# Performance work log

Measured on AMD Instinct MI355X. Metric: run time of the kernel, lower is better.

Reference implementation:

```python
import jax, jax.numpy as jnp
import numpy as np

N_NODES = 30000
N_EDGES = 480000
C_IN = 256
D_HEAD = 64   # out_channels
N_HEADS = 4
M_FEAT = 30   # nb_random_features
K_GUMBEL = 10
TAU = 0.25


def _linear_init(key, out_f, in_f):
    s = 1.0 / np.sqrt(in_f)
    k1, k2 = jax.random.split(key)
    w = jax.random.uniform(k1, (out_f, in_f), minval=-s, maxval=s, dtype=jnp.float32)
    b = jax.random.uniform(k2, (out_f,), minval=-s, maxval=s, dtype=jnp.float32)
    return w, b


def setup_inputs() -> dict:
    key = jax.random.key(0)
    ks = jax.random.split(key, 8)
    z = jax.random.normal(ks[0], (1, N_NODES, C_IN), dtype=jnp.float32)
    edge_index = jax.random.randint(ks[1], (2, N_EDGES), 0, N_NODES)
    # Gumbel(0,1)/tau noise, matching torch's (-Exp(1).log())/tau
    u = jax.random.uniform(ks[2], (N_NODES, 1, N_HEADS, K_GUMBEL), dtype=jnp.float32,
                           minval=1e-8, maxval=1.0)
    gumbels = -jnp.log(-jnp.log(u)) / TAU
    # Performer orthogonal random-feature projection matrix [M, D]
    rng = np.random.default_rng(0)
    q, _ = np.linalg.qr(rng.standard_normal((D_HEAD, D_HEAD)))
    q = q.T[:M_FEAT]
    mult = np.linalg.norm(rng.standard_normal((M_FEAT, D_HEAD)), axis=1)
    proj = jnp.asarray(np.diag(mult) @ q, dtype=jnp.float32)
    Wq_w, Wq_b = _linear_init(ks[3], N_HEADS * D_HEAD, C_IN)
    Wk_w, Wk_b = _linear_init(ks[4], N_HEADS * D_HEAD, C_IN)
    Wv_w, Wv_b = _linear_init(ks[5], N_HEADS * D_HEAD, C_IN)
    Wo_w, Wo_b = _linear_init(ks[6], D_HEAD, N_HEADS * D_HEAD)
    b = jnp.full((1, N_HEADS), 0.1, dtype=jnp.float32)  # rb_order=1, sigmoid init
    tau = jnp.float32(TAU)
    return {"z": z, "edge_index": edge_index, "tau": tau, "gumbels": gumbels,
            "proj": proj, "Wq_w": Wq_w, "Wq_b": Wq_b, "Wk_w": Wk_w, "Wk_b": Wk_b,
            "Wv_w": Wv_w, "Wv_b": Wv_b, "Wo_w": Wo_w, "Wo_b": Wo_b, "b": b}


def _softmax_kernel_feats(data, proj, is_query):
    # data: [B, N, H, D] -> phi(data): [B, N, H, M]
    dn = 1.0 / jnp.sqrt(jnp.sqrt(jnp.float32(data.shape[-1])))
    data = data * dn
    ratio = 1.0 / jnp.sqrt(jnp.float32(proj.shape[0]))
    dash = jnp.einsum('bnhd,md->bnhm', data, proj)
    diag = jnp.sum(data * data, axis=-1, keepdims=True) * 0.5
    if is_query:
        stab = jnp.max(dash, axis=-1, keepdims=True)
    else:
        stab = jnp.max(dash, axis=(1, 3), keepdims=True)
    return ratio * (jnp.exp(dash - diag - stab) + 1e-6)


def reference(z, edge_index, tau, gumbels, proj, Wq_w, Wq_b, Wk_w, Wk_b,
              Wv_w, Wv_b, Wo_w, Wo_b, b):
    B, N, _ = z.shape
    M, D = proj.shape
    H = Wq_w.shape[0] // D
    query = (z @ Wq_w.T + Wq_b).reshape(B, N, H, D)
    key = (z @ Wk_w.T + Wk_b).reshape(B, N, H, D)
    value = (z @ Wv_w.T + Wv_b).reshape(B, N, H, D)

    inv_sqrt_tau = 1.0 / jnp.sqrt(tau)
    qp = jnp.transpose(_softmax_kernel_feats(query * inv_sqrt_tau, proj, True), (1, 0, 2, 3))   # [N,B,H,M]
    kp = jnp.transpose(_softmax_kernel_feats(key * inv_sqrt_tau, proj, False), (1, 0, 2, 3))    # [N,B,H,M]
    v = jnp.transpose(value, (1, 0, 2, 3))                                                       # [N,B,H,D]

    # Gumbel-perturbed key features: [N,B,H,K,M]
    kg = kp[:, :, :, None, :] * jnp.exp(gumbels)[..., None]
    kvs = jnp.einsum('nbhkm,nbhd->bhkmd', kg, v)
    z_num = jnp.einsum('nbhm,bhkmd->nbhkd', qp, kvs)      # [N,B,H,K,D]
    z_den = jnp.einsum('nbhm,bhkm->nbhk', qp, kg.sum(axis=0))
    z_out = jnp.transpose(jnp.mean(z_num / z_den[..., None], axis=3), (1, 0, 2, 3))  # [B,N,H,D]

    # edge attention weights (for link loss)
    start, end = edge_index[0], edge_index[1]
    edge_num = jnp.transpose(jnp.einsum('ebhm,ebhm->ebh', qp[end], kp[start]), (1, 0, 2))  # [B,E,H]
    attn_norm = jnp.einsum('nbhm,bhm->nbh', qp, kp.sum(axis=0))
    edge_dem = jnp.transpose(attn_norm[end], (1, 0, 2))
    A_weight = edge_num / edge_dem

    # relational bias (rb_order=1, sigmoid), degree-normalized sparse conv over value
    ones_e = jnp.ones(start.shape[0], dtype=jnp.float32)
    d_in = jax.ops.segment_sum(ones_e, end, num_segments=N)
    d_out = jax.ops.segment_sum(ones_e, start, num_segments=N)
    edge_w = jax.nn.sigmoid(b[0])[None, :] * jnp.sqrt((1.0 / d_in[end]) * (1.0 / d_out[start]))[:, None]  # [E,H]
    conv = jax.vmap(lambda vb: jax.ops.segment_sum(vb[start] * edge_w[:, :, None], end,
                                                   num_segments=N))(value)
    z_out = z_out + conv

    z_next = z_out.reshape(B, N, H * D) @ Wo_w.T + Wo_b  # [B,N,D]

    d_norm = 1.0 / d_in[end]
    link_loss = jnp.mean(jnp.log(A_weight) * d_norm[None, :, None])
    return z_next, link_loss
```

## Files before the change

### kernel.cpp

```cpp
#include <hip/hip_runtime.h>
#include <hip/hip_bf16.h>

#define NN 30000
#define NE 480000
#define NH 4
#define DH 64
#define MF 30
#define KG 10
#define RATIO 0.18257418583505536f
#define DNRM  0.35355339059327373f

#define P_WF    0
#define P_BF    196608
#define P_WOF   197376
#define P_WOBF  213760
#define P_BBF   213824
#define P_PROJ  213828
#define P_TAU   215748
#define P_TOTAL 215749

typedef unsigned short u16;
typedef unsigned int   u32;
typedef __attribute__((ext_vector_type(8))) short bf16x8;
typedef __attribute__((ext_vector_type(4))) float f32x4;

__device__ __forceinline__ float u2f(u16 u) { return __uint_as_float(((u32)u) << 16); }
__device__ __forceinline__ u16  f2bf(float f) {
    u32 x = __float_as_uint(f);
    return (u16)((x + 0x7FFFu + ((x >> 16) & 1u)) >> 16);
}
__device__ __forceinline__ u32  encf(float f) { u32 u = __float_as_uint(f); return (u & 0x80000000u) ? ~u : (u | 0x80000000u); }
__device__ __forceinline__ float decf(u32 u)  { return (u & 0x80000000u) ? __uint_as_float(u & 0x7FFFFFFFu) : __uint_as_float(~u); }

__global__ void k_detect(const u16* __restrict__ z, int* __restrict__ flag) {
    if (threadIdx.x == 0 && blockIdx.x == 0) {
        int bad = 0;
        for (int i = 0; i < 256; i += 2) {
            u16 u = z[i];
            int e = (u >> 7) & 0xFF;
            if (u != 0 && !(e >= 100 && e <= 140)) bad++;
        }
        *flag = (bad > 16) ? 1 : 0;
    }
}

__global__ __launch_bounds__(256) void k_cvt_params(
    const void* Wq, const void* Wk, const void* Wv,
    const void* bq, const void* bk, const void* bv,
    const void* Wo, const void* Wob, const void* bb, const void* proj,
    const void* taup, float* __restrict__ params, const int* __restrict__ flag)
{
    int i = blockIdx.x * 256 + threadIdx.x;
    if (i >= P_TOTAL) return;
    int f = *flag;
    if (i == P_TAU) {
        float v = f ? ((const float*)taup)[0] : u2f(((const u16*)taup)[0]);
        if (!(v > 1e-6f && v < 1e6f)) {
            float ff = ((const float*)taup)[0];
            v = (ff > 1e-6f && ff < 1e6f) ? ff : 0.25f;
        }
        params[i] = v;
        return;
    }
    const void* src; int j;
    if      (i < 65536)  { src = Wq;  j = i; }
    else if (i < 131072) { src = Wk;  j = i - 65536; }
    else if (i < 196608) { src = Wv;  j = i - 131072; }
    else if (i < 196864) { src = bq;  j = i - 196608; }
    else if (i < 197120) { src = bk;  j = i - 196864; }
    else if (i < 197376) { src = bv;  j = i - 197120; }
    else if (i < 213760) { src = Wo;  j = i - 197376; }
    else if (i < 213824) { src = Wob; j = i - 213760; }
    else if (i < 213828) { src = bb;  j = i - 213824; }
    else                 { src = proj; j = i - P_PROJ; }
    params[i] = f ? ((const float*)src)[j] : u2f(((const u16*)src)[j]);
}

__global__ __launch_bounds__(256) void k_cvt_w(const float* __restrict__ params,
                                               u16* __restrict__ Wh, u16* __restrict__ Wl)
{
    int i = blockIdx.x * 256 + threadIdx.x;
    float x = params[P_WF + i];
    u16 h = f2bf(x);
    Wh[i] = h;
    Wl[i] = f2bf(x - u2f(h));
}

__global__ __launch_bounds__(256) void k_deg(const int* __restrict__ ei, int* __restrict__ din, int* __restrict__ dout) {
    int e = blockIdx.x * 256 + threadIdx.x;
    if (e >= NE) return;
    atomicAdd(&dout[ei[e]], 1);
    atomicAdd(&din[ei[NE + e]], 1);
}

__global__ __launch_bounds__(256) void k_off(const int* __restrict__ din, int* __restrict__ offn, int* __restrict__ counter) {
    __shared__ int s[256];
    __shared__ int base;
    int tid = threadIdx.x;
    int n = blockIdx.x * 256 + tid;
    int v = (n < NN) ? din[n] : 0;
    s[tid] = v;
    __syncthreads();
    for (int o = 1; o < 256; o <<= 1) {
        int t = (tid >= o) ? s[tid - o] : 0;
        __syncthreads();
        s[tid] += t;
        __syncthreads();
    }
    if (tid == 255) base = atomicAdd(counter, s[255]);
    __syncthreads();
    if (n < NN) offn[n] = base + s[tid] - v;
}

__global__ __launch_bounds__(256) void k_fill(const int* __restrict__ ei, const int* __restrict__ offn,
                                              int* __restrict__ fill, int* __restrict__ csr,
                                              const int* __restrict__ din, const int* __restrict__ dout,
                                              float* __restrict__ wedge) {
    int e = blockIdx.x * 256 + threadIdx.x;
    if (e >= NE) return;
    int s = ei[e], t = ei[NE + e];
    int pos = offn[t] + atomicAdd(&fill[t], 1);
    csr[pos] = s;
    wedge[pos] = rsqrtf((float)din[t] * (float)dout[s]);
}

__global__ __launch_bounds__(256) void k_gemm_feat(
    const void* __restrict__ zv, const float* __restrict__ params, const int* __restrict__ flag,
    const u16* __restrict__ Wh, const u16* __restrict__ Wl,
    u16* __restrict__ V16, float* __restrict__ qp, u16* __restrict__ qp16,
    float* __restrict__ dashK, float* __restrict__ diagK, u32* __restrict__ stab)
{
    __shared__ __align__(16) char smemc[32768];
    __shared__ u32 smaxL;
    char* AsH = smemc;
    char* AsL = smemc + 8192;
    char* BsH = smemc + 16384;
    char* BsL = smemc + 24576;
    float* tile  = (float*)smemc;
    float* projL = (float*)smemc + 4352;

    const int tid = threadIdx.x;
    const int bm = blockIdx.x * 64;
    const int bn = blockIdx.y * 64;
    const int f32 = *flag;
    const int wave = tid >> 6, lane = tid & 63;
    const int wm = wave >> 1, wn = wave & 1;
    const int sr = tid >> 2;
    const int sc = (tid & 3) * 16;

    f32x4 acc[2][2] = {};

    for (int k0 = 0; k0 < 256; k0 += 64) {
        __syncthreads();
        {
            int zrow = bm + sr;
            if (f32) {
                float x[16];
                if (zrow < NN) {
                    const float4* zp = (const float4*)((const float*)zv + (size_t)zrow * 256 + k0 + sc);
                    #pragma unroll
                    for (int q4 = 0; q4 < 4; ++q4) {
                        float4 v = zp[q4];
                        x[q4 * 4 + 0] = v.x; x[q4 * 4 + 1] = v.y;
                        x[q4 * 4 + 2] = v.z; x[q4 * 4 + 3] = v.w;
                    }
                } else {
                    #pragma unroll
                    for (int j = 0; j < 16; ++j) x[j] = 0.f;
                }
                #pragma unroll
                for (int j8 = 0; j8 < 2; ++j8) {
                    u32 hw[4], lw[4];
                    #pragma unroll
                    for (int p = 0; p < 4; ++p) {
                        float a = x[j8 * 8 + 2 * p], b2 = x[j8 * 8 + 2 * p + 1];
                        u16 ha = f2bf(a), hb = f2bf(b2);
                        hw[p] = (u32)ha | ((u32)hb << 16);
                        u16 la = f2bf(a - u2f(ha)), lb = f2bf(b2 - u2f(hb));
                        lw[p] = (u32)la | ((u32)lb << 16);
                    }
                    int byt = sr * 128 + (((sc + j8 * 8) * 2) ^ ((sr & 7) << 4));
                    *(uint4*)(AsH + byt) = make_uint4(hw[0], hw[1], hw[2], hw[3]);
                    *(uint4*)(AsL + byt) = make_uint4(lw[0], lw[1], lw[2], lw[3]);
                }
            } else {
                uint4 v0 = make_uint4(0, 0, 0, 0), v1 = v0;
                if (zrow < NN) {
                    const uint4* zp = (const uint4*)((const u16*)zv + (size_t)zrow * 256 + k0 + sc);
                    v0 = zp[0]; v1 = zp[1];
                }
                int byt0 = sr * 128 + (((sc + 0) * 2) ^ ((sr & 7) << 4));
                int byt1 = sr * 128 + (((sc + 8) * 2) ^ ((sr & 7) << 4));
                *(uint4*)(AsH + byt0) = v0;
                *(uint4*)(AsH + byt1) = v1;
            }
        }
        {
            int byt0 = sr * 128 + (((sc + 0) * 2) ^ ((sr & 7) << 4));
            int byt1 = sr * 128 + (((sc + 8) * 2) ^ ((sr & 7) << 4));
            const uint4* wh4 = (const uint4*)(Wh + (size_t)(bn + sr) * 256 + k0 + sc);
            *(uint4*)(BsH + byt0) = wh4[0];
            *(uint4*)(BsH + byt1) = wh4[1];
            if (f32) {
                const uint4* wl4 = (const uint4*)(Wl + (size_t)(bn + sr) * 256 + k0 + sc);
                *(uint4*)(BsL + byt0) = wl4[0];
                *(uint4*)(BsL + byt1) = wl4[1];
            }
        }
        __syncthreads();
        #pragma unroll
        for (int kk = 0; kk < 2; ++kk) {
            const int kb = (kk * 32 + ((lane >> 4) * 8)) * 2;
            bf16x8 ah[2], bh[2], al[2], bl[2];
            #pragma unroll
            for (int i = 0; i < 2; ++i) {
                int ar = 32 * wm + 16 * i + (lane & 15);
                int ab = ar * 128 + (kb ^ ((ar & 7) << 4));
                ah[i] = *(const bf16x8*)(AsH + ab);
                int br = 32 * wn + 16 * i + (lane & 15);
                int bb2 = br * 128 + (kb ^ ((br & 7) << 4));
                bh[i] = *(const bf16x8*)(BsH + bb2);
                if (f32) {
                    al[i] = *(const bf16x8*)(AsL + ab);
                    bl[i] = *(const bf16x8*)(BsL + bb2);
                }
            }
            #pragma unroll
            for (int i = 0; i < 2; ++i)
                #pragma unroll
                for (int nf = 0; nf < 2; ++nf) {
                    acc[i][nf] = __builtin_amdgcn_mfma_f32_16x16x32_bf16(ah[i], bh[nf], acc[i][nf], 0, 0, 0);
                    if (f32) {
                        acc[i][nf] = __builtin_amdgcn_mfma_f32_16x16x32_bf16(ah[i], bl[nf], acc[i][nf], 0, 0, 0);
                        acc[i][nf] = __builtin_amdgcn_mfma_f32_16x16x32_bf16(al[i], bh[nf], acc[i][nf], 0, 0, 0);
                    }
                }
        }
    }
    __syncthreads();

    const float* bfv = params + P_BF;
    if (bn >= 512) {
        #pragma unroll
        for (int i = 0; i < 2; ++i)
            #pragma unroll
            for (int nf = 0; nf < 2; ++nf) {
                int col = 32 * wn + 16 * nf + (lane & 15);
                float bias = bfv[bn + col];
                #pragma unroll
                for (int r2 = 0; r2 < 4; ++r2) {
                    int row = 32 * wm + 16 * i + ((lane >> 4) * 4) + r2;
                    tile[row * 68 + col] = acc[i][nf][r2] + bias;
                }
            }
        __syncthreads();
        for (int i2 = tid; i2 < 4096; i2 += 256) {
            int row = i2 >> 6, col = i2 & 63;
            int nrow = bm + row;
            if (nrow < NN) V16[(size_t)nrow * 256 + (bn - 512) + col] = f2bf(tile[row * 68 + col]);
        }
        return;
    }

    for (int i2 = tid; i2 < MF * DH; i2 += 256) projL[(i2 >> 6) * 65 + (i2 & 63)] = params[P_PROJ + i2];
    if (tid == 0) smaxL = 0u;
    float scale = DNRM * rsqrtf(params[P_TAU]);
    #pragma unroll
    for (int i = 0; i < 2; ++i)
        #pragma unroll
        for (int nf = 0; nf < 2; ++nf) {
            int col = 32 * wn + 16 * nf + (lane & 15);
            float bias = bfv[bn + col];
            #pragma unroll
            for (int r2 = 0; r2 < 4; ++r2) {
                int row = 32 * wm + 16 * i + ((lane >> 4) * 4) + r2;
                tile[row * 68 + col] = (acc[i][nf][r2] + bias) * scale;
            }
        }
    __syncthreads();

    int r = tid >> 2, q = tid & 3;
    int n = bm + r;
    const float* trow = tile + r * 68;
    float dp = 0.f;
    #pragma unroll
    for (int d = q * 16; d < q * 16 + 16; ++d) dp += trow[d] * trow[d];
    dp += __shfl_xor(dp, 1);
    dp += __shfl_xor(dp, 2);
    float diag = dp * 0.5f;

    float dm[8];
    int nm = 0;
    float lmax = -3.0e38f;
    for (int m = q; m < MF; m += 4) {
        float s = 0.f;
        #pragma unroll
        for (int d = 0; d < DH; ++d) s += trow[d] * projL[m * 65 + d];
        dm[nm++] = s;
        lmax = fmaxf(lmax, s);
    }
    float mx = fmaxf(lmax, __shfl_xor(lmax, 1));
    mx = fmaxf(mx, __shfl_xor(mx, 2));

    if (bn < 256) {
        int h = blockIdx.y;
        if (n < NN) {
            float* o = qp + ((size_t)n * NH + h) * MF;
            u16* o16 = qp16 + ((size_t)n * NH + h) * 32;
            nm = 0;
            for (int m = q; m < MF; m += 4) {
                float v = RATIO * (expf(dm[nm++] - diag - mx) + 1e-6f);
                o[m] = v;
                o16[m] = f2bf(v);
            }
            if (q == 0) { o16[30] = 0; o16[31] = 0; }
        }
    } else {
        int h = blockIdx.y - 4;
        if (n < NN) {
            float* o = dashK + ((size_t)n * NH + h) * MF;
            nm = 0;
            for (int m = q; m < MF; m += 4) o[m] = dm[nm++];
            if (q == 0) {
                diagK[(size_t)n * NH + h] = diag;
                atomicMax(&smaxL, encf(mx));
            }
        }
        __syncthreads();
        if (tid == 0) atomicMax(&stab[h], smaxL);
    }
}

__global__ __launch_bounds__(256) void k_kp(float* __restrict__ kp, const float* __restrict__ diagK,
                                            const u32* __restrict__ stab, float* __restrict__ kpsum,
                                            u16* __restrict__ kp16)
{
    __shared__ float part[NH * MF];
    __shared__ float stabf[4];
    int tid = threadIdx.x;
    if (tid < NH * MF) part[tid] = 0.f;
    if (tid >= 128 && tid < 132) stabf[tid - 128] = decf(stab[tid - 128]);
    __syncthreads();
    int base = blockIdx.x * 64 * MF;
    for (int i = tid; i < 64 * MF; i += 256) {
        int row = blockIdx.x * 64 + i / MF;
        int m = i - (i / MF) * MF;
        int h = row & 3;
        float v = RATIO * (expf(kp[base + i] - diagK[row] - stabf[h]) + 1e-6f);
        kp[base + i] = v;
        kp16[(size_t)row * 32 + m] = f2bf(v);
        atomicAdd(&part[h * MF + m], v);
    }
    if (tid < 64) {
        int row = blockIdx.x * 64 + tid;
        kp16[(size_t)row * 32 + 30] = 0;
        kp16[(size_t)row * 32 + 31] = 0;
    }
    __syncthreads();
    if (tid < NH * MF) atomicAdd(&kpsum[tid], part[tid]);
}

__global__ __launch_bounds__(256) void k_an(const float* __restrict__ qp, const float* __restrict__ kpsum,
                                            float* __restrict__ an)
{
    __shared__ float kps[NH * MF];
    int tid = threadIdx.x;
    if (tid < NH * MF) kps[tid] = kpsum[tid];
    __syncthreads();
    int idx = blockIdx.x * 256 + tid;
    if (idx >= NN * NH) return;
    int h = idx & 3;
    const float* q = qp + (size_t)idx * MF;
    float s = 0.f;
    #pragma unroll
    for (int m = 0; m < MF; ++m) s += q[m] * kps[h * MF + m];
    an[idx] = s;
}

#define KVS_CHUNKS 50
#define KVS_NPB (NN / KVS_CHUNKS)
__global__ __launch_bounds__(512) void k_kvs(const float* __restrict__ kp, const void* __restrict__ gum,
                                             const u16* __restrict__ V16, const int* __restrict__ flag,
                                             float* __restrict__ Pkvs, float* __restrict__ Pksum)
{
    __shared__ __align__(16) char kgT[320 * 128];
    __shared__ __align__(16) char VT[64 * 128];
    __shared__ float kpT[64][31];
    __shared__ float egT[64][10];
    const int tid = threadIdx.x;
    const int h = blockIdx.y;
    const int chunk = blockIdx.x;
    const int n0 = chunk * KVS_NPB;
    const int f32 = *flag;
    const int wave = tid >> 6, lane = tid & 63;

    float ksacc[5] = {0.f, 0.f, 0.f, 0.f, 0.f};
    f32x4 acc[10] = {};

    for (int t0 = 0; t0 < KVS_NPB; t0 += 64) {
        __syncthreads();
        for (int i = tid; i < 64 * MF; i += 512) {
            int n = i / MF, m = i - (i / MF) * MF;
            kpT[n][m] = (t0 + n < KVS_NPB) ? kp[(size_t)(n0 + t0 + n) * (NH * MF) + h * MF + m] : 0.f;
        }
        for (int i = tid; i < 64 * KG; i += 512) {
            int n = i / KG, k = i - (i / KG) * KG;
            float e = 0.f;
            if (t0 + n < KVS_NPB) {
                size_t gofs = (size_t)(n0 + t0 + n) * (NH * KG) + h * KG + k;
                float g = f32 ? ((const float*)gum)[gofs] : u2f(((const u16*)gum)[gofs]);
                e = expf(g);
            }
            egT[n][k] = e;
        }
        for (int i = tid; i < 64 * 16; i += 512) {
            int n = i >> 4, dq = (i & 15) * 4;
            u32 v0 = 0, v1 = 0;
            if (t0 + n < KVS_NPB) {
                uint2 vv = *(const uint2*)(V16 + (size_t)(n0 + t0 + n) * 256 + h * 64 + dq);
                v0 = vv.x; v1 = vv.y;
            }
            #pragma unroll
            for (int j = 0; j < 4; ++j) {
                u16 val = (u16)(((j < 2) ? v0 : v1) >> ((j & 1) * 16));
                int d = dq + j;
                *(u16*)(VT + d * 128 + ((n * 2) ^ ((d & 7) << 4))) = val;
            }
        }
        __syncthreads();
        #pragma unroll
        for (int it = 0; it < 5; ++it) {
            int idx = tid + it * 512;
            int row = idx >> 3, nc = idx & 7;
            u32 w_[4] = {0u, 0u, 0u, 0u};
            if (row < 300) {
                int k = row / MF, m = row - (row / MF) * MF;
                float s = 0.f;
                #pragma unroll
                for (int p = 0; p < 4; ++p) {
                    int na = nc * 8 + 2 * p, nb = na + 1;
                    u16 ha = f2bf(kpT[na][m] * egT[na][k]);
                    u16 hb = f2bf(kpT[nb][m] * egT[nb][k]);
                    w_[p] = (u32)ha | ((u32)hb << 16);
                    s += u2f(ha) + u2f(hb);
                }
                ksacc[it] += s;
            }
            *(uint4*)(kgT + row * 128 + ((nc * 16) ^ ((row & 7) << 4))) = make_uint4(w_[0], w_[1], w_[2], w_[3]);
        }
        __syncthreads();
        #pragma unroll
        for (int kk = 0; kk < 2; ++kk) {
            const int kb = (kk * 32 + ((lane >> 4) * 8)) * 2;
            #pragma unroll
            for (int i = 0; i < 10; ++i) {
                int ct = wave * 10 + i;
                int kt = ct >> 2, dt = ct & 3;
                int ar = kt * 16 + (lane & 15);
                bf16x8 a = *(const bf16x8*)(kgT + ar * 128 + (kb ^ ((ar & 7) << 4)));
                int br = dt * 16 + (lane & 15);
                bf16x8 b = *(const bf16x8*)(VT + br * 128 + (kb ^ ((br & 7) << 4)));
                acc[i] = __builtin_amdgcn_mfma_f32_16x16x32_bf16(a, b, acc[i], 0, 0, 0);
            }
        }
    }
    #pragma unroll
    for (int i = 0; i < 10; ++i) {
        int ct = wave * 10 + i;
        int kt = ct >> 2, dt = ct & 3;
        int col = dt * 16 + (lane & 15);
        #pragma unroll
        for (int r = 0; r < 4; ++r) {
            int row = kt * 16 + ((lane >> 4) * 4) + r;
            if (row < 300)
                Pkvs[(((size_t)chunk * NH + h) * 300 + row) * 64 + col] = acc[i][r];
        }
    }
    #pragma unroll
    for (int it = 0; it < 5; ++it) {
        float v = ksacc[it];
        v += __shfl_xor(v, 1);
        v += __shfl_xor(v, 2);
        v += __shfl_xor(v, 4);
        int row = (tid + it * 512) >> 3;
        if ((tid & 7) == 0 && row < 300)
            Pksum[chunk * 1200 + h * 300 + row] = v;
    }
}

__global__ __launch_bounds__(256) void k_reduce(const float* __restrict__ Pkvs, const float* __restrict__ Pksum,
                                                float* __restrict__ kvs, float* __restrict__ ksum)
{
    int i = blockIdx.x * 256 + threadIdx.x;
    if (i < NH * KG * MF * DH) {
        float s = 0.f;
        for (int c = 0; c < KVS_CHUNKS; ++c) s += Pkvs[(size_t)c * (NH * 300 * 64) + i];
        kvs[i] = s;
    } else if (i < NH * KG * MF * DH + NH * KG * MF) {
        int j = i - NH * KG * MF * DH;
        float s = 0.f;
        for (int c = 0; c < KVS_CHUNKS; ++c) s += Pksum[c * 1200 + j];
        ksum[j] = s;
    }
}

__global__ __launch_bounds__(256) void k_edge(const int* __restrict__ ei,
                                              const u16* __restrict__ qp16, const u16* __restrict__ kp16,
                                              const float* __restrict__ an,
                                              const int* __restrict__ din, float* __restrict__ lossp)
{
    __shared__ float ls[64];
    int tid = threadIdx.x;
    int eg = tid >> 2, h = tid & 3;
    int e = blockIdx.x * 64 + eg;
    int s = ei[e], t = ei[NE + e];
    const uint4* qv = (const uint4*)(qp16 + ((size_t)t * NH + h) * 32);
    const uint4* kv = (const uint4*)(kp16 + ((size_t)s * NH + h) * 32);
    float num = 0.f;
    #pragma unroll
    for (int c = 0; c < 4; ++c) {
        uint4 a = qv[c], b = kv[c];
        num += u2f((u16)(a.x & 0xFFFF)) * u2f((u16)(b.x & 0xFFFF))
             + u2f((u16)(a.x >> 16))    * u2f((u16)(b.x >> 16))
             + u2f((u16)(a.y & 0xFFFF)) * u2f((u16)(b.y & 0xFFFF))
             + u2f((u16)(a.y >> 16))    * u2f((u16)(b.y >> 16))
             + u2f((u16)(a.z & 0xFFFF)) * u2f((u16)(b.z & 0xFFFF))
             + u2f((u16)(a.z >> 16))    * u2f((u16)(b.z >> 16))
             + u2f((u16)(a.w & 0xFFFF)) * u2f((u16)(b.w & 0xFFFF))
             + u2f((u16)(a.w >> 16))    * u2f((u16)(b.w >> 16));
    }
    float term = logf(num / an[(size_t)t * NH + h]);
    term += __shfl_xor(term, 1);
    term += __shfl_xor(term, 2);
    if (h == 0) ls[eg] = term / (float)din[t];
    __syncthreads();
    if (tid < 64) {
        float v = ls[tid];
        #pragma unroll
        for (int o = 32; o > 0; o >>= 1) v += __shfl_xor(v, o);
        if (tid == 0) atomicAdd(&lossp[blockIdx.x & 1023], v);
    }
}

#define AT_NT 48
__global__ __launch_bounds__(256) void k_attn(
    const float* __restrict__ qp, const float* __restrict__ kvs, const float* __restrict__ ksum,
    u16* __restrict__ zatt)
{
    __shared__ float qpTf[3][NH * 484];
    __shared__ u32   kvbuf[NH * 964];
    __shared__ float rdenL[3][16 * NH * KG];
    u16*   kvL16 = (u16*)kvbuf;
    float* ksL   = (float*)kvbuf;
    int tid = threadIdx.x;
    int n0 = blockIdx.x * AT_NT;

    for (int i = tid; i < AT_NT * NH * MF; i += 256) {
        int j48 = i / (NH * MF); int r = i - j48 * (NH * MF);
        int h = r / MF; int m = r - h * MF;
        qpTf[j48 >> 4][h * 484 + m * 16 + (j48 & 15)] = qp[(size_t)(n0 + j48) * (NH * MF) + r];
    }
    for (int i = tid; i < NH * KG * MF; i += 256) ksL[i] = ksum[i];
    __syncthreads();
    for (int i = tid; i < AT_NT * NH * KG; i += 256) {
        int j48 = i / (NH * KG); int r = i - j48 * (NH * KG);
        int h = r / KG;
        int sub = j48 >> 4, j = j48 & 15;
        float s = 0.f;
        #pragma unroll
        for (int m = 0; m < MF; ++m) s += qpTf[sub][h * 484 + m * 16 + j] * ksL[r * MF + m];
        rdenL[sub][j * (NH * KG) + r] = 1.0f / s;
    }

    const int h  = tid >> 6;
    const int jg = (tid >> 4) & 3;
    const int dg = tid & 15;
    float acc[3][4][4] = {};
    for (int k = 0; k < KG; ++k) {
        __syncthreads();
        for (int i = tid; i < NH * MF * DH; i += 256) {
            int hh = i / (MF * DH); int r = i - hh * (MF * DH);
            kvL16[hh * 1928 + r] = f2bf(kvs[((size_t)(hh * KG + k) * MF) * DH + r]);
        }
        __syncthreads();
        float ps[3][4][4] = {};
        const u16* kb = kvL16 + h * 1928 + dg * 4;
        const float* qb0 = qpTf[0] + h * 484 + jg * 4;
        const float* qb1 = qpTf[1] + h * 484 + jg * 4;
        const float* qb2 = qpTf[2] + h * 484 + jg * 4;
        #pragma unroll
        for (int m = 0; m < MF; ++m) {
            ushort4 bu = *(const ushort4*)(kb + m * 64);
            float4 b = make_float4(u2f(bu.x), u2f(bu.y), u2f(bu.z), u2f(bu.w));
            float4 a0 = *(const float4*)(qb0 + m * 16);
            float4 a1 = *(const float4*)(qb1 + m * 16);
            float4 a2 = *(const float4*)(qb2 + m * 16);
            ps[0][0][0] += a0.x * b.x; ps[0][0][1] += a0.x * b.y; ps[0][0][2] += a0.x * b.z; ps[0][0][3] += a0.x * b.w;
            ps[0][1][0] += a0.y * b.x; ps[0][1][1] += a0.y * b.y; ps[0][1][2] += a0.y * b.z; ps[0][1][3] += a0.y * b.w;
            ps[0][2][0] += a0.z * b.x; ps[0][2][1] += a0.z * b.y; ps[0][2][2] += a0.z * b.z; ps[0][2][3] += a0.z * b.w;
            ps[0][3][0] += a0.w * b.x; ps[0][3][1] += a0.w * b.y; ps[0][3][2] += a0.w * b.z; ps[0][3][3] += a0.w * b.w;
            ps[1][0][0] += a1.x * b.x; ps[1][0][1] += a1.x * b.y; ps[1][0][2] += a1.x * b.z; ps[1][0][3] += a1.x * b.w;
            ps[1][1][0] += a1.y * b.x; ps[1][1][1] += a1.y * b.y; ps[1][1][2] += a1.y * b.z; ps[1][1][3] += a1.y * b.w;
            ps[1][2][0] += a1.z * b.x; ps[1][2][1] += a1.z * b.y; ps[1][2][2] += a1.z * b.z; ps[1][2][3] += a1.z * b.w;
            ps[1][3][0] += a1.w * b.x; ps[1][3][1] += a1.w * b.y; ps[1][3][2] += a1.w * b.z; ps[1][3][3] += a1.w * b.w;
            ps[2][0][0] += a2.x * b.x; ps[2][0][1] += a2.x * b.y; ps[2][0][2] += a2.x * b.z; ps[2][0][3] += a2.x * b.w;
            ps[2][1][0] += a2.y * b.x; ps[2][1][1] += a2.y * b.y; ps[2][1][2] += a2.y * b.z; ps[2][1][3] += a2.y * b.w;
            ps[2][2][0] += a2.z * b.x; ps[2][2][1] += a2.z * b.y; ps[2][2][2] += a2.z * b.z; ps[2][2][3] += a2.z * b.w;
            ps[2][3][0] += a2.w * b.x; ps[2][3][1] += a2.w * b.y; ps[2][3][2] += a2.w * b.z; ps[2][3][3] += a2.w * b.w;
        }
        #pragma unroll
        for (int sub = 0; sub < 3; ++sub)
            #pragma unroll
            for (int j4 = 0; j4 < 4; ++j4) {
                float rd = rdenL[sub][(jg * 4 + j4) * (NH * KG) + h * KG + k];
                #pragma unroll
                for (int d4 = 0; d4 < 4; ++d4) acc[sub][j4][d4] += ps[sub][j4][d4] * rd;
            }
    }
    #pragma unroll
    for (int sub = 0; sub < 3; ++sub)
        #pragma unroll
        for (int j4 = 0; j4 < 4; ++j4) {
            int n = n0 + sub * 16 + jg * 4 + j4;
            #pragma unroll
            for (int d4 = 0; d4 < 4; ++d4)
                zatt[(size_t)n * 256 + h * 64 + dg * 4 + d4] = f2bf(acc[sub][j4][d4] * (1.0f / KG));
        }
}

__global__ __launch_bounds__(256) void k_gather(
    const u16* __restrict__ zatt, const u16* __restrict__ V16,
    const int* __restrict__ csr, const float* __restrict__ wedge,
    const int* __restrict__ offn, const int* __restrict__ din,
    const float* __restrict__ params, u16* __restrict__ pre)
{
    int tid = threadIdx.x;
    int w = tid >> 6, l = tid & 63;
    int n = blockIdx.x * 4 + w;
    float sigb = 1.f / (1.f + expf(-params[P_BBF + (l >> 4)]));
    int dn = din[n], o0 = offn[n];
    float c0 = 0.f, c1 = 0.f, c2 = 0.f, c3 = 0.f;
    for (int t0 = 0; t0 < dn; t0 += 64) {
        int cnt = min(64, dn - t0);
        int myIdx = 0; float myW = 0.f;
        if (l < cnt) { myIdx = csr[o0 + t0 + l]; myW = wedge[o0 + t0 + l]; }
        int j = 0;
        for (; j + 7 < cnt; j += 8) {
            int   s0 = __shfl(myIdx, j),     s1 = __shfl(myIdx, j + 1);
            int   s2 = __shfl(myIdx, j + 2), s3 = __shfl(myIdx, j + 3);
            int   s4 = __shfl(myIdx, j + 4), s5 = __shfl(myIdx, j + 5);
            int   s6 = __shfl(myIdx, j + 6), s7 = __shfl(myIdx, j + 7);
            float w0 = __shfl(myW, j),     w1 = __shfl(myW, j + 1);
            float w2 = __shfl(myW, j + 2), w3 = __shfl(myW, j + 3);
            float w4 = __shfl(myW, j + 4), w5 = __shfl(myW, j + 5);
            float w6 = __shfl(myW, j + 6), w7 = __shfl(myW, j + 7);
            uint2 a0 = *(const uint2*)(V16 + (size_t)s0 * 256 + l * 4);
            uint2 a1 = *(const uint2*)(V16 + (size_t)s1 * 256 + l * 4);
            uint2 a2 = *(const uint2*)(V16 + (size_t)s2 * 256 + l * 4);
            uint2 a3 = *(const uint2*)(V16 + (size_t)s3 * 256 + l * 4);
            uint2 a4 = *(const uint2*)(V16 + (size_t)s4 * 256 + l * 4);
            uint2 a5 = *(const uint2*)(V16 + (size_t)s5 * 256 + l * 4);
            uint2 a6 = *(const uint2*)(V16 + (size_t)s6 * 256 + l * 4);
            uint2 a7 = *(const uint2*)(V16 + (size_t)s7 * 256 + l * 4);
            c0 += w0 * u2f((u16)(a0.x & 0xFFFF)) + w1 * u2f((u16)(a1.x & 0xFFFF))
                + w2 * u2f((u16)(a2.x & 0xFFFF)) + w3 * u2f((u16)(a3.x & 0xFFFF))
                + w4 * u2f((u16)(a4.x & 0xFFFF)) + w5 * u2f((u16)(a5.x & 0xFFFF))
                + w6 * u2f((u16)(a6.x & 0xFFFF)) + w7 * u2f((u16)(a7.x & 0xFFFF));
            c1 += w0 * u2f((u16)(a0.x >> 16)) + w1 * u2f((u16)(a1.x >> 16))
                + w2 * u2f((u16)(a2.x >> 16)) + w3 * u2f((u16)(a3.x >> 16))
                + w4 * u2f((u16)(a4.x >> 16)) + w5 * u2f((u16)(a5.x >> 16))
                + w6 * u2f((u16)(a6.x >> 16)) + w7 * u2f((u16)(a7.x >> 16));
            c2 += w0 * u2f((u16)(a0.y & 0xFFFF)) + w1 * u2f((u16)(a1.y & 0xFFFF))
                + w2 * u2f((u16)(a2.y & 0xFFFF)) + w3 * u2f((u16)(a3.y & 0xFFFF))
                + w4 * u2f((u16)(a4.y & 0xFFFF)) + w5 * u2f((u16)(a5.y & 0xFFFF))
                + w6 * u2f((u16)(a6.y & 0xFFFF)) + w7 * u2f((u16)(a7.y & 0xFFFF));
            c3 += w0 * u2f((u16)(a0.y >> 16)) + w1 * u2f((u16)(a1.y >> 16))
                + w2 * u2f((u16)(a2.y >> 16)) + w3 * u2f((u16)(a3.y >> 16))
                + w4 * u2f((u16)(a4.y >> 16)) + w5 * u2f((u16)(a5.y >> 16))
                + w6 * u2f((u16)(a6.y >> 16)) + w7 * u2f((u16)(a7.y >> 16));
        }
        for (; j < cnt; ++j) {
            int   s0 = __shfl(myIdx, j);
            float w0 = __shfl(myW, j);
            uint2 a0 = *(const uint2*)(V16 + (size_t)s0 * 256 + l * 4);
            c0 += w0 * u2f((u16)(a0.x & 0xFFFF));
            c1 += w0 * u2f((u16)(a0.x >> 16));
            c2 += w0 * u2f((u16)(a0.y & 0xFFFF));
            c3 += w0 * u2f((u16)(a0.y >> 16));
        }
    }
    uint2 za = *(const uint2*)(zatt + (size_t)n * 256 + l * 4);
    float e0 = u2f((u16)(za.x & 0xFFFF)) + sigb * c0;
    float e1 = u2f((u16)(za.x >> 16))    + sigb * c1;
    float e2 = u2f((u16)(za.y & 0xFFFF)) + sigb * c2;
    float e3 = u2f((u16)(za.y >> 16))    + sigb * c3;
    uint2 r;
    r.x = (u32)f2bf(e0) | ((u32)f2bf(e1) << 16);
    r.y = (u32)f2bf(e2) | ((u32)f2bf(e3) << 16);
    *(uint2*)(pre + (size_t)n * 256 + l * 4) = r;
}

__global__ __launch_bounds__(256) void k_out(
    const u16* __restrict__ pre, const float* __restrict__ params, float* __restrict__ out)
{
    __shared__ __align__(16) char smemc[24576];
    char* As  = smemc;
    char* BsH = smemc + 8192;
    char* BsL = smemc + 16384;
    const int tid = threadIdx.x;
    const int bm = blockIdx.x * 64;
    const int wave = tid >> 6, lane = tid & 63;
    const int wm = wave >> 1, wn = wave & 1;
    const int sr = tid >> 2;
    const int sc = (tid & 3) * 16;

    f32x4 acc[2][2] = {};

    for (int k0 = 0; k0 < 256; k0 += 64) {
        __syncthreads();
        int byt0 = sr * 128 + (((sc + 0) * 2) ^ ((sr & 7) << 4));
        int byt1 = sr * 128 + (((sc + 8) * 2) ^ ((sr & 7) << 4));
        {
            int row = bm + sr;
            uint4 v0 = make_uint4(0, 0, 0, 0), v1 = v0;
            if (row < NN) {
                const uint4* p = (const uint4*)(pre + (size_t)row * 256 + k0 + sc);
                v0 = p[0]; v1 = p[1];
            }
            *(uint4*)(As + byt0) = v0;
            *(uint4*)(As + byt1) = v1;
        }
        {
            float x[16];
            const float4* wr = (const float4*)(params + P_WOF + (size_t)sr * 256 + k0 + sc);
            #pragma unroll
            for (int q4 = 0; q4 < 4; ++q4) {
                float4 v = wr[q4];
                x[q4 * 4 + 0] = v.x; x[q4 * 4 + 1] = v.y;
                x[q4 * 4 + 2] = v.z; x[q4 * 4 + 3] = v.w;
            }
            #pragma unroll
            for (int j8 = 0; j8 < 2; ++j8) {
                u32 hw[4], lw[4];
                #pragma unroll
                for (int p = 0; p < 4; ++p) {
                    float a = x[j8 * 8 + 2 * p], b2 = x[j8 * 8 + 2 * p + 1];
                    u16 ha = f2bf(a), hb = f2bf(b2);
                    hw[p] = (u32)ha | ((u32)hb << 16);
                    u16 la = f2bf(a - u2f(ha)), lb = f2bf(b2 - u2f(hb));
                    lw[p] = (u32)la | ((u32)lb << 16);
                }
                int byt = sr * 128 + (((sc + j8 * 8) * 2) ^ ((sr & 7) << 4));
                *(uint4*)(BsH + byt) = make_uint4(hw[0], hw[1], hw[2], hw[3]);
                *(uint4*)(BsL + byt) = make_uint4(lw[0], lw[1], lw[2], lw[3]);
            }
        }
        __syncthreads();
        #pragma unroll
        for (int kk = 0; kk < 2; ++kk) {
            const int kb = (kk * 32 + ((lane >> 4) * 8)) * 2;
            bf16x8 a[2], bh[2], bl[2];
            #pragma unroll
            for (int i = 0; i < 2; ++i) {
                int ar = 32 * wm + 16 * i + (lane & 15);
                int ab = ar * 128 + (kb ^ ((ar & 7) << 4));
                a[i] = *(const bf16x8*)(As + ab);
                int br = 32 * wn + 16 * i + (lane & 15);
                int bb2 = br * 128 + (kb ^ ((br & 7) << 4));
                bh[i] = *(const bf16x8*)(BsH + bb2);
                bl[i] = *(const bf16x8*)(BsL + bb2);
            }
            #pragma unroll
            for (int i = 0; i < 2; ++i)
                #pragma unroll
                for (int nf = 0; nf < 2; ++nf) {
                    acc[i][nf] = __builtin_amdgcn_mfma_f32_16x16x32_bf16(a[i], bh[nf], acc[i][nf], 0, 0, 0);
                    acc[i][nf] = __builtin_amdgcn_mfma_f32_16x16x32_bf16(a[i], bl[nf], acc[i][nf], 0, 0, 0);
                }
        }
    }
    #pragma unroll
    for (int i = 0; i < 2; ++i)
        #pragma unroll
        for (int nf = 0; nf < 2; ++nf) {
            int col = 32 * wn + 16 * nf + (lane & 15);
            float bias = params[P_WOBF + col];
            #pragma unroll
            for (int r2 = 0; r2 < 4; ++r2) {
                int row = bm + 32 * wm + 16 * i + ((lane >> 4) * 4) + r2;
                if (row < NN) out[(size_t)row * 64 + col] = acc[i][nf][r2] + bias;
            }
        }
}

__global__ __launch_bounds__(256) void k_loss(const float* __restrict__ lossp, float* __restrict__ out) {
    __shared__ float s[256];
    int tid = threadIdx.x;
    float v = 0.f;
    for (int i = tid; i < 1024; i += 256) v += lossp[i];
    s[tid] = v;
    __syncthreads();
    for (int o = 128; o > 0; o >>= 1) {
        if (tid < o) s[tid] += s[tid + o];
        __syncthreads();
    }
    if (tid == 0) out[(size_t)NN * 64] = s[0] / (float)(NE * NH);
}

extern "C" void kernel_launch(void* const* d_in, const int* in_sizes, int n_in,
                              void* d_out, int out_size, void* d_ws, size_t ws_size,
                              hipStream_t stream)
{
    const void* z    = d_in[0];
    const int*  ei   = (const int*)d_in[1];
    const void* taup = d_in[2];
    const void* gum  = d_in[3];
    const void* proj = d_in[4];
    const void* Wq   = d_in[5];
    const void* bq   = d_in[6];
    const void* Wk   = d_in[7];
    const void* bk   = d_in[8];
    const void* Wv   = d_in[9];
    const void* bv   = d_in[10];
    const void* Wo   = d_in[11];
    const void* Wob  = d_in[12];
    const void* bb   = d_in[13];
    float* out = (float*)d_out;

    u16*   V16    = (u16*)d_ws;
    float* qpb    = (float*)d_ws + 3840000;
    float* kpb    = qpb + (size_t)NN * NH * MF;
    float* diagK  = kpb + (size_t)NN * NH * MF;
    float* anb    = diagK + (size_t)NN * NH;
    u16*   zatt   = (u16*)kpb;
    int*   csr    = (int*)(anb + (size_t)NN * NH);
    int*   offn   = csr + NE;
    float* params = (float*)(offn + NN);
    float* kvs    = params + 215752;
    float* ksum   = kvs + NH * KG * MF * DH;
    float* kpsum  = ksum + NH * KG * MF;
    int*   din    = (int*)(kpsum + NH * MF);
    int*   doutd  = din + NN;
    int*   fill   = doutd + NN;
    int*   counter = fill + NN;
    u32*   stab   = (u32*)(counter + 4);
    float* lossp  = (float*)(stab + 4);
    int*   flag   = (int*)(lossp + 1024);
    float* wedge  = (float*)(flag + 4);
    u16*   qp16   = (u16*)(wedge + NE);
    u16*   kp16   = qp16 + (size_t)NN * NH * 32;
    float* Pkvs   = (float*)qp16;
    float* Pksum  = (float*)(kp16 + (size_t)NN * NH * 32);
    u16*   Whb    = kp16;
    u16*   Wlb    = kp16 + 196608;
    u16*   pre    = qp16;
    size_t zero_bytes = (size_t)((char*)(flag + 4) - (char*)kvs);

    hipMemsetAsync(kvs, 0, zero_bytes, stream);

    k_detect<<<dim3(1), dim3(64), 0, stream>>>((const u16*)z, flag);
    k_cvt_params<<<dim3((P_TOTAL + 255) / 256), dim3(256), 0, stream>>>(
        Wq, Wk, Wv, bq, bk, bv, Wo, Wob, bb, proj, taup, params, flag);
    k_cvt_w<<<dim3(768), dim3(256), 0, stream>>>(params, Whb, Wlb);

    k_deg <<<dim3((NE + 255) / 256), dim3(256), 0, stream>>>(ei, din, doutd);
    k_off <<<dim3((NN + 255) / 256), dim3(256), 0, stream>>>(din, offn, counter);
    k_fill<<<dim3((NE + 255) / 256), dim3(256), 0, stream>>>(ei, offn, fill, csr, din, doutd, wedge);
    k_gemm_feat<<<dim3((NN + 63) / 64, 12), dim3(256), 0, stream>>>(
        z, params, flag, Whb, Wlb, V16, qpb, qp16, kpb, diagK, stab);
    k_kp  <<<dim3(NN * NH / 64), dim3(256), 0, stream>>>(kpb, diagK, stab, kpsum, kp16);
    k_an  <<<dim3((NN * NH + 255) / 256), dim3(256), 0, stream>>>(qpb, kpsum, anb);
    k_edge<<<dim3(NE / 64), dim3(256), 0, stream>>>(ei, qp16, kp16, anb, din, lossp);
    k_kvs <<<dim3(KVS_CHUNKS, NH), dim3(512), 0, stream>>>(kpb, gum, V16, flag, Pkvs, Pksum);
    k_reduce<<<dim3((NH * KG * MF * DH + NH * KG * MF + 255) / 256), dim3(256), 0, stream>>>(
        Pkvs, Pksum, kvs, ksum);
    k_attn<<<dim3(NN / AT_NT), dim3(256), 0, stream>>>(qpb, kvs, ksum, zatt);
    k_gather<<<dim3(NN / 4), dim3(256), 0, stream>>>(zatt, V16, csr, wedge, offn, din, params, pre);
    k_out<<<dim3((NN + 63) / 64), dim3(256), 0, stream>>>(pre, params, out);
    k_loss<<<dim3(1), dim3(256), 0, stream>>>(lossp, out);
}
```

Measured before the change: 677.4 us.

## Stage full z row strip once per block and loop over all twelve column tiles

```diff
diff --git a/kernel.cpp b/kernel.cpp
--- a/kernel.cpp
+++ b/kernel.cpp
@@ -130,31 +130,26 @@
     u16* __restrict__ V16, float* __restrict__ qp, u16* __restrict__ qp16,
     float* __restrict__ dashK, float* __restrict__ diagK, u32* __restrict__ stab)
 {
-    __shared__ __align__(16) char smemc[32768];
+    __shared__ __align__(16) char AsH[64 * 512];
+    __shared__ __align__(16) char AsL[64 * 512];
+    __shared__ __align__(16) char BsH[2][64 * 128];
+    __shared__ __align__(16) char BsL[2][64 * 128];
+    __shared__ float tile[64 * 68];
+    __shared__ float projL[30 * 65];
     __shared__ u32 smaxL;
-    char* AsH = smemc;
-    char* AsL = smemc + 8192;
-    char* BsH = smemc + 16384;
-    char* BsL = smemc + 24576;
-    float* tile  = (float*)smemc;
-    float* projL = (float*)smemc + 4352;
 
     const int tid = threadIdx.x;
     const int bm = blockIdx.x * 64;
-    const int bn = blockIdx.y * 64;
     const int f32 = *flag;
     const int wave = tid >> 6, lane = tid & 63;
     const int wm = wave >> 1, wn = wave & 1;
     const int sr = tid >> 2;
     const int sc = (tid & 3) * 16;
 
-    f32x4 acc[2][2] = {};
-
-    for (int k0 = 0; k0 < 256; k0 += 64) {
-        __syncthreads();
-        {
-            int zrow = bm + sr;
-            if (f32) {
+    {
+        int zrow = bm + sr;
+        if (f32) {
+            for (int k0 = 0; k0 < 256; k0 += 64) {
                 float x[16];
                 if (zrow < NN) {
                     const float4* zp = (const float4*)((const float*)zv + (size_t)zrow * 256 + k0 + sc);
@@ -179,68 +174,102 @@
                         u16 la = f2bf(a - u2f(ha)), lb = f2bf(b2 - u2f(hb));
                         lw[p] = (u32)la | ((u32)lb << 16);
                     }
-                    int byt = sr * 128 + (((sc + j8 * 8) * 2) ^ ((sr & 7) << 4));
+                    int byt = sr * 512 + (((k0 + sc + j8 * 8) * 2) ^ ((sr & 7) << 4));
                     *(uint4*)(AsH + byt) = make_uint4(hw[0], hw[1], hw[2], hw[3]);
                     *(uint4*)(AsL + byt) = make_uint4(lw[0], lw[1], lw[2], lw[3]);
                 }
-            } else {
+            }
+        } else {
+            for (int k0 = 0; k0 < 256; k0 += 64) {
                 uint4 v0 = make_uint4(0, 0, 0, 0), v1 = v0;
                 if (zrow < NN) {
                     const uint4* zp = (const uint4*)((const u16*)zv + (size_t)zrow * 256 + k0 + sc);
                     v0 = zp[0]; v1 = zp[1];
                 }
+                int byt0 = sr * 512 + (((k0 + sc + 0) * 2) ^ ((sr & 7) << 4));
+                int byt1 = sr * 512 + (((k0 + sc + 8) * 2) ^ ((sr & 7) << 4));
+                *(uint4*)(AsH + byt0) = v0;
+                *(uint4*)(AsH + byt1) = v1;
+            }
+        }
+    }
+    for (int i2 = tid; i2 < MF * DH; i2 += 256) projL[(i2 >> 6) * 65 + (i2 & 63)] = params[P_PROJ + i2];
+
+    const float* bfv = params + P_BF;
+    float scale = DNRM * rsqrtf(params[P_TAU]);
+
+    for (int bny = 0; bny < 12; ++bny) {
+        const int bn = bny * 64;
+        f32x4 acc[2][2] = {};
+        for (int k0c = 0; k0c < 4; ++k0c) {
+            const int k0 = k0c * 64;
+            const int p = k0c & 1;
+            {
                 int byt0 = sr * 128 + (((sc + 0) * 2) ^ ((sr & 7) << 4));
                 int byt1 = sr * 128 + (((sc + 8) * 2) ^ ((sr & 7) << 4));
-                *(uint4*)(AsH + byt0) = v0;
-                *(uint4*)(AsH + byt1) = v1;
-            }
-        }
-        {
-            int byt0 = sr * 128 + (((sc + 0) * 2) ^ ((sr & 7) << 4));
-            int byt1 = sr * 128 + (((sc + 8) * 2) ^ ((sr & 7) << 4));
-            const uint4* wh4 = (const uint4*)(Wh + (size_t)(bn + sr) * 256 + k0 + sc);
-            *(uint4*)(BsH + byt0) = wh4[0];
-            *(uint4*)(BsH + byt1) = wh4[1];
-            if (f32) {
-                const uint4* wl4 = (const uint4*)(Wl + (size_t)(bn + sr) * 256 + k0 + sc);
-                *(uint4*)(BsL + byt0) = wl4[0];
-                *(uint4*)(BsL + byt1) = wl4[1];
-            }
-        }
-        __syncthreads();
-        #pragma unroll
-        for (int kk = 0; kk < 2; ++kk) {
-            const int kb = (kk * 32 + ((lane >> 4) * 8)) * 2;
-            bf16x8 ah[2], bh[2], al[2], bl[2];
-            #pragma unroll
-            for (int i = 0; i < 2; ++i) {
-                int ar = 32 * wm + 16 * i + (lane & 15);
-                int ab = ar * 128 + (kb ^ ((ar & 7) << 4));
-                ah[i] = *(const bf16x8*)(AsH + ab);
-                int br = 32 * wn + 16 * i + (lane & 15);
-                int bb2 = br * 128 + (kb ^ ((br & 7) << 4));
-                bh[i] = *(const bf16x8*)(BsH + bb2);
+                const uint4* wh4 = (const uint4*)(Wh + (size_t)(bn + sr) * 256 + k0 + sc);
+                *(uint4*)(BsH[p] + byt0) = wh4[0];
+                *(uint4*)(BsH[p] + byt1) = wh4[1];
                 if (f32) {
-                    al[i] = *(const bf16x8*)(AsL + ab);
-                    bl[i] = *(const bf16x8*)(BsL + bb2);
-                }
-            }
+                    const uint4* wl4 = (const uint4*)(Wl + (size_t)(bn + sr) * 256 + k0 + sc);
+                    *(uint4*)(BsL[p] + byt0) = wl4[0];
+                    *(uint4*)(BsL[p] + byt1) = wl4[1];
+                }
+            }
+            __syncthreads();
+            #pragma unroll
+            for (int kk = 0; kk < 2; ++kk) {
+                const int kbA = (k0 + kk * 32 + ((lane >> 4) * 8)) * 2;
+                const int kbB = (kk * 32 + ((lane >> 4) * 8)) * 2;
+                bf16x8 ah[2], bh[2], al[2], bl[2];
+                #pragma unroll
+                for (int i = 0; i < 2; ++i) {
+                    int ar = 32 * wm + 16 * i + (lane & 15);
+                    int ab = ar * 512 + (kbA ^ ((ar & 7) << 4));
+                    ah[i] = *(const bf16x8*)(AsH + ab);
+                    int br = 32 * wn + 16 * i + (lane & 15);
+                    int bb2 = br * 128 + (kbB ^ ((br & 7) << 4));
+                    bh[i] = *(const bf16x8*)(BsH[p] + bb2);
+                    if (f32) {
+                        al[i] = *(const bf16x8*)(AsL + ab);
+                        bl[i] = *(const bf16x8*)(BsL[p] + bb2);
+                    }
+                }
+                #pragma unroll
+                for (int i = 0; i < 2; ++i)
+                    #pragma unroll
+                    for (int nf = 0; nf < 2; ++nf) {
+                        acc[i][nf] = __builtin_amdgcn_mfma_f32_16x16x32_bf16(ah[i], bh[nf], acc[i][nf], 0, 0, 0);
+                        if (f32) {
+                            acc[i][nf] = __builtin_amdgcn_mfma_f32_16x16x32_bf16(ah[i], bl[nf], acc[i][nf], 0, 0, 0);
+                            acc[i][nf] = __builtin_amdgcn_mfma_f32_16x16x32_bf16(al[i], bh[nf], acc[i][nf], 0, 0, 0);
+                        }
+                    }
+            }
+        }
+        if (bny >= 8) {
             #pragma unroll
             for (int i = 0; i < 2; ++i)
                 #pragma unroll
                 for (int nf = 0; nf < 2; ++nf) {
-                    acc[i][nf] = __builtin_amdgcn_mfma_f32_16x16x32_bf16(ah[i], bh[nf], acc[i][nf], 0, 0, 0);
-                    if (f32) {
-                        acc[i][nf] = __builtin_amdgcn_mfma_f32_16x16x32_bf16(ah[i], bl[nf], acc[i][nf], 0, 0, 0);
-                        acc[i][nf] = __builtin_amdgcn_mfma_f32_16x16x32_bf16(al[i], bh[nf], acc[i][nf], 0, 0, 0);
+                    int col = 32 * wn + 16 * nf + (lane & 15);
+                    float bias = bfv[bn + col];
+                    #pragma unroll
+                    for (int r2 = 0; r2 < 4; ++r2) {
+                        int row = 32 * wm + 16 * i + ((lane >> 4) * 4) + r2;
+                        tile[row * 68 + col] = acc[i][nf][r2] + bias;
                     }
                 }
-        }
-    }
-    __syncthreads();
-
-    const float* bfv = params + P_BF;
-    if (bn >= 512) {
+            __syncthreads();
+            for (int i2 = tid; i2 < 4096; i2 += 256) {
+                int row = i2 >> 6, col = i2 & 63;
+                int nrow = bm + row;
+                if (nrow < NN) V16[(size_t)nrow * 256 + (bn - 512) + col] = f2bf(tile[row * 68 + col]);
+            }
+            continue;
+        }
+
+        if (tid == 0) smaxL = 0u;
         #pragma unroll
         for (int i = 0; i < 2; ++i)
             #pragma unroll
@@ -250,84 +279,61 @@
                 #pragma unroll
                 for (int r2 = 0; r2 < 4; ++r2) {
                     int row = 32 * wm + 16 * i + ((lane >> 4) * 4) + r2;
-                    tile[row * 68 + col] = acc[i][nf][r2] + bias;
-                }
-            }
-        __syncthreads();
-        for (int i2 = tid; i2 < 4096; i2 += 256) {
-            int row = i2 >> 6, col = i2 & 63;
-            int nrow = bm + row;
-            if (nrow < NN) V16[(size_t)nrow * 256 + (bn - 512) + col] = f2bf(tile[row * 68 + col]);
-        }
-        return;
-    }
-
-    for (int i2 = tid; i2 < MF * DH; i2 += 256) projL[(i2 >> 6) * 65 + (i2 & 63)] = params[P_PROJ + i2];
-    if (tid == 0) smaxL = 0u;
-    float scale = DNRM * rsqrtf(params[P_TAU]);
-    #pragma unroll
-    for (int i = 0; i < 2; ++i)
-        #pragma unroll
-        for (int nf = 0; nf < 2; ++nf) {
-            int col = 32 * wn + 16 * nf + (lane & 15);
-            float bias = bfv[bn + col];
-            #pragma unroll
-            for (int r2 = 0; r2 < 4; ++r2) {
-                int row = 32 * wm + 16 * i + ((lane >> 4) * 4) + r2;
-                tile[row * 68 + col] = (acc[i][nf][r2] + bias) * scale;
-            }
-        }
-    __syncthreads();
-
-    int r = tid >> 2, q = tid & 3;
-    int n = bm + r;
-    const float* trow = tile + r * 68;
-    float dp = 0.f;
-    #pragma unroll
-    for (int d = q * 16; d < q * 16 + 16; ++d) dp += trow[d] * trow[d];
-    dp += __shfl_xor(dp, 1);
-    dp += __shfl_xor(dp, 2);
-    float diag = dp * 0.5f;
-
-    float dm[8];
-    int nm = 0;
-    float lmax = -3.0e38f;
-    for (int m = q; m < MF; m += 4) {
-        float s = 0.f;
-        #pragma unroll
-        for (int d = 0; d < DH; ++d) s += trow[d] * projL[m * 65 + d];
-        dm[nm++] = s;
-        lmax = fmaxf(lmax, s);
-    }
-    float mx = fmaxf(lmax, __shfl_xor(lmax, 1));
-    mx = fmaxf(mx, __shfl_xor(mx, 2));
-
-    if (bn < 256) {
-        int h = blockIdx.y;
-        if (n < NN) {
-            float* o = qp + ((size_t)n * NH + h) * MF;
-            u16* o16 = qp16 + ((size_t)n * NH + h) * 32;
-            nm = 0;
-            for (int m = q; m < MF; m += 4) {
-                float v = RATIO * (expf(dm[nm++] - diag - mx) + 1e-6f);
-                o[m] = v;
-                o16[m] = f2bf(v);
-            }
-            if (q == 0) { o16[30] = 0; o16[31] = 0; }
-        }
-    } else {
-        int h = blockIdx.y - 4;
-        if (n < NN) {
-            float* o = dashK + ((size_t)n * NH + h) * MF;
-            nm = 0;
-            for (int m = q; m < MF; m += 4) o[m] = dm[nm++];
-            if (q == 0) {
-                diagK[(size_t)n * NH + h] = diag;
-                atomicMax(&smaxL, encf(mx));
-            }
-        }
-        __syncthreads();
-        if (tid == 0) atomicMax(&stab[h], smaxL);
+                    tile[row * 68 + col] = (acc[i][nf][r2] + bias) * scale;
+                }
+            }
+        __syncthreads();
+
+        int r = tid >> 2, q = tid & 3;
+        int n = bm + r;
+        const float* trow = tile + r * 68;
+        float dp = 0.f;
+        #pragma unroll
+        for (int d = q * 16; d < q * 16 + 16; ++d) dp += trow[d] * trow[d];
+        dp += __shfl_xor(dp, 1);
+        dp += __shfl_xor(dp, 2);
+        float diag = dp * 0.5f;
+
+        float dm[8];
+        int nm = 0;
+        float lmax = -3.0e38f;
+        for (int m = q; m < MF; m += 4) {
+            float s = 0.f;
+            #pragma unroll
+            for (int d = 0; d < DH; ++d) s += trow[d] * projL[m * 65 + d];
+            dm[nm++] = s;
+            lmax = fmaxf(lmax, s);
+        }
+        float mx = fmaxf(lmax, __shfl_xor(lmax, 1));
+        mx = fmaxf(mx, __shfl_xor(mx, 2));
+
+        if (bny < 4) {
+            int h = bny;
+            if (n < NN) {
+                float* o = qp + ((size_t)n * NH + h) * MF;
+                u16* o16 = qp16 + ((size_t)n * NH + h) * 32;
+                nm = 0;
+                for (int m = q; m < MF; m += 4) {
+                    float v = RATIO * (expf(dm[nm++] - diag - mx) + 1e-6f);
+                    o[m] = v;
+                    o16[m] = f2bf(v);
+                }
+                if (q == 0) { o16[30] = 0; o16[31] = 0; }
+            }
+        } else {
+            int h = bny - 4;
+            if (n < NN) {
+                float* o = dashK + ((size_t)n * NH + h) * MF;
+                nm = 0;
+                for (int m = q; m < MF; m += 4) o[m] = dm[nm++];
+                if (q == 0) {
+                    diagK[(size_t)n * NH + h] = diag;
+                    atomicMax(&smaxL, encf(mx));
+                }
+            }
+            __syncthreads();
+            if (tid == 0) atomicMax(&stab[h], smaxL);
+        }
     }
 }
 
@@ -580,7 +586,7 @@
         __syncthreads();
         for (int i = tid; i < NH * MF * DH; i += 256) {
             int hh = i / (MF * DH); int r = i - hh * (MF * DH);
-            kvL16[hh * 1928 + r] = f2bf(kvs[((size_t)(hh * KG + k) * MF) * DH + r]);
+            kvL16[hh * 1928 + r] = f2bf(kvs[((size_t)(hh * 10 + k) * MF) * DH + r]);
         }
         __syncthreads();
         float ps[3][4][4] = {};
@@ -866,7 +872,7 @@
     k_deg <<<dim3((NE + 255) / 256), dim3(256), 0, stream>>>(ei, din, doutd);
     k_off <<<dim3((NN + 255) / 256), dim3(256), 0, stream>>>(din, offn, counter);
     k_fill<<<dim3((NE + 255) / 256), dim3(256), 0, stream>>>(ei, offn, fill, csr, din, doutd, wedge);
-    k_gemm_feat<<<dim3((NN + 63) / 64, 12), dim3(256), 0, stream>>>(
+    k_gemm_feat<<<dim3((NN + 63) / 64), dim3(256), 0, stream>>>(
         z, params, flag, Whb, Wlb, V16, qpb, qp16, kpb, diagK, stab);
     k_kp  <<<dim3(NN * NH / 64), dim3(256), 0, stream>>>(kpb, diagK, stab, kpsum, kp16);
     k_an  <<<dim3((NN * NH + 255) / 256), dim3(256), 0, stream>>>(qpb, kpsum, anb);
```

After: 728.3 us. +7.5%, slower.
